# Performance work log

Measured on AMD Instinct MI355X. Metric: run time of the kernel, lower is better.

Reference implementation:

```python
import jax, jax.numpy as jnp
import numpy as np

B, N, C = 8, 8192, 256
H, D, S = 8, 32, 32          # heads, dim_head, slice_num
HID = 4 * C                  # mlp hidden


def layernorm(x, w, b, eps=1e-5):
    mu = jnp.mean(x, axis=-1, keepdims=True)
    var = jnp.mean(jnp.square(x - mu), axis=-1, keepdims=True)
    return (x - mu) * jax.lax.rsqrt(var + eps) * w + b


def setup_inputs() -> dict:
    key = jax.random.key(0)
    ks = jax.random.split(key, 16)
    s = lambda fan: 1.0 / np.sqrt(fan)
    return {
        "fx": jax.random.normal(ks[0], (B, N, C), jnp.float32),
        "ln1_w": jnp.ones((C,), jnp.float32),
        "ln1_b": jnp.zeros((C,), jnp.float32),
        "Wx": jax.random.uniform(ks[1], (C, C), jnp.float32, -s(C), s(C)),   # in_project_x weight [inner,dim]
        "bx": jax.random.uniform(ks[2], (C,), jnp.float32, -s(C), s(C)),
        "Wq": jax.random.uniform(ks[3], (S, D), jnp.float32, -s(D), s(D)),
        "Wk": jax.random.uniform(ks[4], (S, D), jnp.float32, -s(D), s(D)),
        "Wv": jax.random.uniform(ks[5], (D, D), jnp.float32, -s(D), s(D)),
        "Wo": jax.random.uniform(ks[6], (C, C), jnp.float32, -s(C), s(C)),   # to_out weight [dim,inner]
        "bo": jax.random.uniform(ks[7], (C,), jnp.float32, -s(C), s(C)),
        "ln2_w": jnp.ones((C,), jnp.float32),
        "ln2_b": jnp.zeros((C,), jnp.float32),
        "W1": jax.random.uniform(ks[8], (HID, C), jnp.float32, -s(C), s(C)),
        "b1": jax.random.uniform(ks[9], (HID,), jnp.float32, -s(C), s(C)),
        "W2": jax.random.uniform(ks[10], (C, HID), jnp.float32, -s(HID), s(HID)),
        "b2": jax.random.uniform(ks[11], (C,), jnp.float32, -s(HID), s(HID)),
    }


def linear_no_attn(x, Wx, bx, Wq, Wk, Wv, Wo, bo):
    # x: [B,N,C]
    x_mid = x @ Wx.T + bx                                   # [B,N,C]
    x_mid = x_mid.reshape(x.shape[0], x.shape[1], H, D).transpose(0, 2, 1, 3)  # [B,H,N,D]
    q = jax.nn.softmax(x_mid @ Wq.T, axis=-1)               # [B,H,N,S], softmax over slices
    k = jax.nn.softmax(x_mid @ Wk.T, axis=-2)               # [B,H,N,S], softmax over tokens
    v = x_mid @ Wv.T                                        # [B,H,N,D]
    kv = jnp.einsum('bhns,bhnd->bhsd', k, v)                # [B,H,S,D]
    qkv = jnp.einsum('bhns,bhsd->bhnd', q, kv)              # [B,H,N,D]
    qkv = qkv.transpose(0, 2, 1, 3).reshape(x.shape[0], x.shape[1], H * D)
    return qkv @ Wo.T + bo


def reference(fx, ln1_w, ln1_b, Wx, bx, Wq, Wk, Wv, Wo, bo, ln2_w, ln2_b, W1, b1, W2, b2):
    h = linear_no_attn(layernorm(fx, ln1_w, ln1_b), Wx, bx, Wq, Wk, Wv, Wo, bo) + fx
    y = layernorm(h, ln2_w, ln2_b)
    y = jax.nn.gelu(y @ W1.T + b1, approximate=False)       # MLP: pre + exact GELU, n_layers=0
    y = y @ W2.T + b2
    return y + h
```

## Files before the change

### kernel.cpp

```cpp
#include <hip/hip_runtime.h>
#include <math.h>


typedef __attribute__((ext_vector_type(8))) short bf8;
typedef __attribute__((ext_vector_type(4))) float f32x4;
typedef __attribute__((ext_vector_type(4))) unsigned short u16x4;
typedef __attribute__((ext_vector_type(8))) unsigned short u16x8;

__device__ __forceinline__ float b2f(unsigned short x) {
  union { unsigned u; float f; } t; t.u = ((unsigned)x) << 16; return t.f;
}
__device__ __forceinline__ unsigned short f2b(float f) {
  union { float f; unsigned u; } t; t.f = f;
  unsigned r = t.u + 0x7fffu + ((t.u >> 16) & 1u);
  return (unsigned short)(r >> 16);
}
__device__ __forceinline__ float gelu_exact(float x) {
  return 0.5f * x * (1.0f + erff(x * 0.7071067811865475f));
}
__device__ __forceinline__ float erf_fast(float x) {
  float ax = fabsf(x);
  float t = __builtin_amdgcn_rcpf(fmaf(0.3275911f, ax, 1.0f));
  float p = t * fmaf(t, fmaf(t, fmaf(t, fmaf(t, 1.061405429f, -1.453152027f),
                                     1.421413741f), -0.284496736f), 0.254829592f);
  float r = 1.0f - p * __expf(-ax * ax);
  return copysignf(r, x);
}
__device__ __forceinline__ float gelu_fast(float x) {
  return 0.5f * x * (1.0f + erf_fast(x * 0.7071067811865475f));
}

typedef __attribute__((address_space(1))) const void gas_void;
typedef __attribute__((address_space(3))) void las_void;
__device__ __forceinline__ void gl_lds16(const void* g, void* l) {
  __builtin_amdgcn_global_load_lds((gas_void*)g, (las_void*)l, 16, 0, 0);
}

__global__ void sniff_kernel(const unsigned* __restrict__ fx, int* __restrict__ flag) {
  if (threadIdx.x == 0) {
    int cnt = 0;
    for (int i = 0; i < 64; i++) {
      unsigned e = (fx[i] >> 7) & 0xFFu;
      cnt += (e >= 117u && e <= 130u) ? 1 : 0;
    }
    *flag = (cnt >= 32) ? 1 : 0;
  }
}

struct CvtDesc { const void* src[15]; int off[15]; int n[15]; };

__global__ __launch_bounds__(256) void cvt_tab(CvtDesc d, unsigned short* __restrict__ wtab,
                                               const int* __restrict__ flagp) {
  const int seg = blockIdx.y;
  const int i = blockIdx.x * 256 + threadIdx.x;
  if (i >= d.n[seg]) return;
  unsigned short o;
  if (*flagp) o = ((const unsigned short*)d.src[seg])[i];
  else        o = f2b(((const float*)d.src[seg])[i]);
  wtab[d.off[seg] + i] = o;
}

__global__ __launch_bounds__(256) void build_big(
    const unsigned short* __restrict__ wq, const unsigned short* __restrict__ wk,
    unsigned short* __restrict__ Wqbig, unsigned short* __restrict__ Wkbig)
{
  const int idx = blockIdx.x * 256 + threadIdx.x;
  const int row = idx >> 8, col = idx & 255;
  const bool same = (row >> 5) == (col >> 5);
  const int wi = (row & 31) * 32 + (col & 31);
  Wqbig[idx] = same ? wq[wi] : (unsigned short)0;
  Wkbig[idx] = same ? wk[wi] : (unsigned short)0;
}

__global__ __launch_bounds__(256) void zero_u16(unsigned short* __restrict__ p, int n) {
  int i8 = (blockIdx.x * 256 + threadIdx.x) * 8;
  if (i8 < n) { u16x8 z = {}; *(u16x8*)&p[i8] = z; }
}

__global__ __launch_bounds__(256) void ln_stats(
    const void* __restrict__ X, const int* __restrict__ flagp, int amode,
    float* __restrict__ MU, float* __restrict__ RS)
{
  const int lane = threadIdx.x & 63;
  const int wave = threadIdx.x >> 6;
  const size_t row = (size_t)blockIdx.x * 4 + wave;
  const size_t base = row * 256 + lane * 4;
  const bool abf = amode ? ((*flagp) != 0) : true;
  float x0, x1, x2, x3;
  if (abf) {
    u16x4 uv = *(const u16x4*)&((const unsigned short*)X)[base];
    x0 = b2f(uv[0]); x1 = b2f(uv[1]); x2 = b2f(uv[2]); x3 = b2f(uv[3]);
  } else {
    f32x4 t = *(const f32x4*)&((const float*)X)[base];
    x0 = t[0]; x1 = t[1]; x2 = t[2]; x3 = t[3];
  }
  float s = x0 + x1 + x2 + x3;
  float q = x0*x0 + x1*x1 + x2*x2 + x3*x3;
  #pragma unroll
  for (int m = 1; m < 64; m <<= 1) { s += __shfl_xor(s, m, 64); q += __shfl_xor(q, m, 64); }
  float mean = s * (1.0f / 256.0f);
  float var  = q * (1.0f / 256.0f) - mean * mean;
  if (lane == 0) { MU[row] = mean; RS[row] = rsqrtf(var + 1e-5f); }
}

__global__ __launch_bounds__(256) void gemm_bt(
    const unsigned short* __restrict__ A,
    const unsigned short* __restrict__ W,
    const unsigned short* __restrict__ bias,
    const void* __restrict__ Res, const int* __restrict__ flagp,
    unsigned short* __restrict__ Y,
    int N, int K, int act, int mz, long wz)
{
  __shared__ __align__(16) unsigned short smem[3 * 8192];
  const int tid = threadIdx.x, lane = tid & 63, wave = tid >> 6;
  const size_t zrow = (size_t)blockIdx.z * mz;
  const int bm = blockIdx.x * 128, bn = blockIdx.y * 128;
  const int wm = (wave >> 1) * 64, wn = (wave & 1) * 64;
  const int quad = lane >> 4, l16 = lane & 15;
  const unsigned short* Wz = W + (size_t)blockIdx.z * wz;

  f32x4 acc[4][4] = {};
  const int r0 = tid >> 2;
  const int co = (tid & 3) * 8;
  const unsigned short* pa0 = &A[(zrow + bm + r0) * K + co];
  const unsigned short* pa1 = &A[(zrow + bm + r0 + 64) * K + co];
  const unsigned short* pb0 = &Wz[(size_t)(bn + r0) * K + co];
  const unsigned short* pb1 = &Wz[(size_t)(bn + r0 + 64) * K + co];
  const int nt = K >> 5;

  auto stage = [&](int t, int sl) {
    const int k0 = t << 5;
    unsigned short* b_ = &smem[sl * 8192 + tid * 8];
    gl_lds16(pa0 + k0, b_);
    gl_lds16(pa1 + k0, b_ + 2048);
    gl_lds16(pb0 + k0, b_ + 4096);
    gl_lds16(pb1 + k0, b_ + 6144);
  };

  stage(0, 0);
  if (nt > 1) stage(1, 1);
  int scur = 0, snew = 2;
  for (int t = 0; t < nt; ++t) {
    if (t + 2 < nt) {
      stage(t + 2, snew);
      asm volatile("s_waitcnt vmcnt(8)" ::: "memory");
    } else if (t + 1 < nt) {
      asm volatile("s_waitcnt vmcnt(4)" ::: "memory");
    } else {
      asm volatile("s_waitcnt vmcnt(0)" ::: "memory");
    }
    __builtin_amdgcn_s_barrier();
    __builtin_amdgcn_sched_barrier(0);

    const unsigned short* sa = &smem[scur * 8192];
    const unsigned short* sb = sa + 4096;
    bf8 af[4], bfr[4];
    #pragma unroll
    for (int i = 0; i < 4; i++) af[i]  = *(const bf8*)&sa[(wm + i * 16 + l16) * 32 + quad * 8];
    #pragma unroll
    for (int j = 0; j < 4; j++) bfr[j] = *(const bf8*)&sb[(wn + j * 16 + l16) * 32 + quad * 8];
    #pragma unroll
    for (int i = 0; i < 4; i++)
      #pragma unroll
      for (int j = 0; j < 4; j++)
        acc[i][j] = __builtin_amdgcn_mfma_f32_16x16x32_bf16(af[i], bfr[j], acc[i][j], 0, 0, 0);

    __builtin_amdgcn_sched_barrier(0);
    __builtin_amdgcn_s_barrier();
    scur = scur + 1 < 3 ? scur + 1 : 0;
    snew = snew + 1 < 3 ? snew + 1 : 0;
  }

  const bool rbf = Res ? ((*flagp) != 0) : true;
  float bv[4];
  #pragma unroll
  for (int j = 0; j < 4; j++) bv[j] = b2f(bias[bn + wn + j * 16 + l16]);
  #pragma unroll
  for (int i = 0; i < 4; i++)
    #pragma unroll
    for (int j = 0; j < 4; j++)
      #pragma unroll
      for (int r = 0; r < 4; r++) {
        float v = acc[i][j][r] + bv[j];
        if (act == 2) v = __expf(v);
        acc[i][j][r] = v;
      }
  if (act == 3) {
    #pragma unroll
    for (int i = 0; i < 4; i++)
      #pragma unroll
      for (int g = 0; g < 2; g++)
        #pragma unroll
        for (int r = 0; r < 4; r++) {
          float a0 = acc[i][2*g][r], a1 = acc[i][2*g+1][r];
          float m = fmaxf(a0, a1);
          #pragma unroll
          for (int msk = 1; msk < 16; msk <<= 1) m = fmaxf(m, __shfl_xor(m, msk, 64));
          float e0 = __expf(a0 - m), e1 = __expf(a1 - m);
          float s = e0 + e1;
          #pragma unroll
          for (int msk = 1; msk < 16; msk <<= 1) s += __shfl_xor(s, msk, 64);
          const float rz = 1.0f / s;
          acc[i][2*g][r] = e0 * rz; acc[i][2*g+1][r] = e1 * rz;
        }
  }

  float* cf = (float*)smem;
  const int whalf = wm >> 6;
  #pragma unroll
  for (int half = 0; half < 2; ++half) {
    __builtin_amdgcn_s_barrier();
    if (whalf == half) {
      #pragma unroll
      for (int i = 0; i < 4; i++)
        #pragma unroll
        for (int j = 0; j < 4; j++)
          #pragma unroll
          for (int r = 0; r < 4; r++)
            cf[(i * 16 + quad * 4 + r) * 128 + wn + j * 16 + l16] = acc[i][j][r];
    }
    __builtin_amdgcn_s_barrier();
    #pragma unroll
    for (int st = 0; st < 4; ++st) {
      const int e = st * 2048 + tid * 8;
      const int row = e >> 7;
      const size_t gbase = (zrow + bm + half * 64 + row) * (size_t)N + bn + (e & 127);
      float v[8];
      #pragma unroll
      for (int u = 0; u < 8; u++) v[u] = cf[e + u];
      if (Res) {
        if (rbf) {
          u16x8 rv = *(const u16x8*)&((const unsigned short*)Res)[gbase];
          #pragma unroll
          for (int u = 0; u < 8; u++) v[u] += b2f(rv[u]);
        } else {
          f32x4 ra = *(const f32x4*)&((const float*)Res)[gbase];
          f32x4 rb = *(const f32x4*)&((const float*)Res)[gbase + 4];
          v[0] += ra[0]; v[1] += ra[1]; v[2] += ra[2]; v[3] += ra[3];
          v[4] += rb[0]; v[5] += rb[1]; v[6] += rb[2]; v[7] += rb[3];
        }
      }
      u16x8 o;
      #pragma unroll
      for (int u = 0; u < 8; u++) o[u] = f2b(v[u]);
      *(u16x8*)&Y[gbase] = o;
    }
  }
}

__global__ __launch_bounds__(256) void gemm_bt_ln(
    const void* __restrict__ A, const int* __restrict__ flagp, int amode,
    const float* __restrict__ MU, const float* __restrict__ RS,
    const unsigned short* __restrict__ lw, const unsigned short* __restrict__ lb,
    const unsigned short* __restrict__ W, const unsigned short* __restrict__ bias,
    unsigned short* __restrict__ Y, int N, int K, int act)
{
  __shared__ __align__(16) unsigned char smemc[32768];
  unsigned short* lA = (unsigned short*)smemc;
  unsigned short* lB = lA + 4096;
  const int tid = threadIdx.x, lane = tid & 63, wave = tid >> 6;
  const int bm = blockIdx.x * 128, bn = blockIdx.y * 128;
  const int wm = (wave >> 1) * 64, wn = (wave & 1) * 64;
  const int quad = lane >> 4, l16 = lane & 15;
  const bool abf = amode ? ((*flagp) != 0) : true;
  const unsigned short* Ab = (const unsigned short*)A;
  const float* Af = (const float*)A;

  f32x4 acc[4][4] = {};
  const int r0 = tid >> 2;
  const int co = (tid & 3) * 8;
  const unsigned short* pb0 = &W[(size_t)(bn + r0) * K + co];
  const unsigned short* pb1 = &W[(size_t)(bn + r0 + 64) * K + co];

  for (int k0 = 0; k0 < K; k0 += 32) {
    u16x8 wv8 = *(const u16x8*)&lw[k0 + co];
    u16x8 bv8 = *(const u16x8*)&lb[k0 + co];
    __syncthreads();
    gl_lds16(pb0 + k0, &lB[tid * 8]);
    gl_lds16(pb1 + k0, &lB[2048 + tid * 8]);
    #pragma unroll
    for (int half = 0; half < 2; half++) {
      const int ar = bm + r0 + half * 64;
      const float m_ = MU[ar], r_ = RS[ar];
      float xv[8];
      if (abf) {
        u16x8 t = *(const u16x8*)&Ab[(size_t)ar * K + k0 + co];
        #pragma unroll
        for (int e = 0; e < 8; e++) xv[e] = b2f(t[e]);
      } else {
        f32x4 t0 = *(const f32x4*)&Af[(size_t)ar * K + k0 + co];
        f32x4 t1 = *(const f32x4*)&Af[(size_t)ar * K + k0 + co + 4];
        xv[0]=t0[0]; xv[1]=t0[1]; xv[2]=t0[2]; xv[3]=t0[3];
        xv[4]=t1[0]; xv[5]=t1[1]; xv[6]=t1[2]; xv[7]=t1[3];
      }
      u16x8 o;
      #pragma unroll
      for (int e = 0; e < 8; e++)
        o[e] = f2b((xv[e] - m_) * r_ * b2f(wv8[e]) + b2f(bv8[e]));
      *(u16x8*)&lA[half * 2048 + tid * 8] = o;
    }
    __syncthreads();

    bf8 af[4], bfr[4];
    #pragma unroll
    for (int i = 0; i < 4; i++) af[i]  = *(const bf8*)&lA[(wm + i * 16 + l16) * 32 + quad * 8];
    #pragma unroll
    for (int j = 0; j < 4; j++) bfr[j] = *(const bf8*)&lB[(wn + j * 16 + l16) * 32 + quad * 8];
    #pragma unroll
    for (int i = 0; i < 4; i++)
      #pragma unroll
      for (int j = 0; j < 4; j++)
        acc[i][j] = __builtin_amdgcn_mfma_f32_16x16x32_bf16(af[i], bfr[j], acc[i][j], 0, 0, 0);
  }

  float bv[4];
  #pragma unroll
  for (int j = 0; j < 4; j++) bv[j] = b2f(bias[bn + wn + j * 16 + l16]);
  #pragma unroll
  for (int i = 0; i < 4; i++)
    #pragma unroll
    for (int j = 0; j < 4; j++)
      #pragma unroll
      for (int r = 0; r < 4; r++) {
        float v = acc[i][j][r] + bv[j];
        if (act) v = gelu_exact(v);
        acc[i][j][r] = v;
      }

  float* cf = (float*)smemc;
  const int whalf = wm >> 6;
  #pragma unroll
  for (int half = 0; half < 2; ++half) {
    __syncthreads();
    if (whalf == half) {
      #pragma unroll
      for (int i = 0; i < 4; i++)
        #pragma unroll
        for (int j = 0; j < 4; j++)
          #pragma unroll
          for (int r = 0; r < 4; r++)
            cf[(i * 16 + quad * 4 + r) * 128 + wn + j * 16 + l16] = acc[i][j][r];
    }
    __syncthreads();
    #pragma unroll
    for (int st = 0; st < 4; ++st) {
      const int e = st * 2048 + tid * 8;
      const int row = e >> 7;
      const size_t gbase = (size_t)(bm + half * 64 + row) * N + bn + (e & 127);
      u16x8 o;
      #pragma unroll
      for (int u = 0; u < 8; u++) o[u] = f2b(cf[e + u]);
      *(u16x8*)&Y[gbase] = o;
    }
  }
}

__global__ __launch_bounds__(256) void fused_mlp(
    const unsigned short* __restrict__ Hsrc,
    const float* __restrict__ MU, const float* __restrict__ RS,
    const unsigned short* __restrict__ lw, const unsigned short* __restrict__ lb,
    const unsigned short* __restrict__ W1, const unsigned short* __restrict__ bs1,
    const unsigned short* __restrict__ W2, const unsigned short* __restrict__ bs2,
    void* __restrict__ OUT, const int* __restrict__ flagp, long row0)
{
  __shared__ __align__(16) unsigned char smem[70656];
  const int tid = threadIdx.x, lane = tid & 63, wave = tid >> 6;
  const int quad = lane >> 4, l16 = lane & 15;
  const int brow = blockIdx.x * 64;

  auto stageW1 = [&](int c, int b) {
    const unsigned short* src = W1 + (size_t)c * 8192;
    unsigned char* dst = smem + b * 16384;
    #pragma unroll
    for (int s = 0; s < 4; s++) {
      const int unit = s * 256 + tid;
      const int row = unit >> 5, u = unit & 31;
      gl_lds16(src + row * 256 + ((u ^ (row & 7)) * 8), dst + unit * 16);
    }
  };
  auto stageW2 = [&](int c, int b) {
    const unsigned short* src = W2 + c * 32;
    unsigned char* dst = smem + 32768 + b * 16384;
    #pragma unroll
    for (int s = 0; s < 4; s++) {
      const int unit = s * 256 + tid;
      const int row = unit >> 2, u = unit & 3;
      gl_lds16(src + (size_t)row * 1024 + ((u ^ ((row >> 1) & 3)) * 8), dst + unit * 16);
    }
  };

  stageW1(0, 0);
  stageW2(0, 0);

  const int myrow = wave * 16 + l16;
  const float m_ = MU[brow + myrow], r_ = RS[brow + myrow];
  const unsigned short* hr = Hsrc + (size_t)(brow + myrow) * 256 + quad * 8;
  bf8 areg[8];
  #pragma unroll
  for (int ks = 0; ks < 8; ks++) {
    u16x8 hv = *(const u16x8*)&hr[ks * 32];
    u16x8 wv = *(const u16x8*)&lw[ks * 32 + quad * 8];
    u16x8 bv = *(const u16x8*)&lb[ks * 32 + quad * 8];
    u16x8 o;
    #pragma unroll
    for (int e = 0; e < 8; e++)
      o[e] = f2b((b2f(hv[e]) - m_) * r_ * b2f(wv[e]) + b2f(bv[e]));
    *(u16x8*)&areg[ks] = o;
  }

  asm volatile("s_waitcnt vmcnt(0)" ::: "memory");
  __builtin_amdgcn_s_barrier();

  f32x4 acc[16] = {};
  unsigned short* tw = (unsigned short*)(smem + 65536 + wave * 1280);
  const int gsw = (l16 >> 1) & 3;
  int bsel = 0;

  for (int c = 0; c < 32; ++c) {
    if (c + 1 < 32) {
      stageW1(c + 1, bsel ^ 1);
      stageW2(c + 1, bsel ^ 1);
      __builtin_amdgcn_sched_barrier(0);
    }

    const unsigned short* w1b = (const unsigned short*)(smem + bsel * 16384);
    f32x4 p0 = {}, p1 = {};
    #pragma unroll
    for (int ks = 0; ks < 8; ks++) {
      const int slot = (ks * 4 + quad) ^ (l16 & 7);
      bf8 a0, a1;
      *(u16x8*)&a0 = *(const u16x8*)&w1b[l16 * 256 + slot * 8];
      *(u16x8*)&a1 = *(const u16x8*)&w1b[(16 + l16) * 256 + slot * 8];
      p0 = __builtin_amdgcn_mfma_f32_16x16x32_bf16(a0, areg[ks], p0, 0, 0, 0);
      p1 = __builtin_amdgcn_mfma_f32_16x16x32_bf16(a1, areg[ks], p1, 0, 0, 0);
    }

    {
      u16x4 bv0 = *(const u16x4*)&bs1[c * 32 + quad * 4];
      u16x4 bv1 = *(const u16x4*)&bs1[c * 32 + 16 + quad * 4];
      u16x4 o0, o1;
      #pragma unroll
      for (int r = 0; r < 4; r++) {
        o0[r] = f2b(gelu_fast(p0[r] + b2f(bv0[r])));
        o1[r] = f2b(gelu_fast(p1[r] + b2f(bv1[r])));
      }
      *(u16x4*)&tw[l16 * 40 + quad * 4]      = o0;
      *(u16x4*)&tw[l16 * 40 + 16 + quad * 4] = o1;
    }
    asm volatile("s_waitcnt lgkmcnt(0)" ::: "memory");
    __builtin_amdgcn_sched_barrier(0);

    bf8 ta;
    *(u16x8*)&ta = *(const u16x8*)&tw[l16 * 40 + quad * 8];
    const unsigned short* w2b = (const unsigned short*)(smem + 32768 + bsel * 16384);
    #pragma unroll
    for (int j = 0; j < 16; j++) {
      bf8 bw;
      *(u16x8*)&bw = *(const u16x8*)&w2b[(j * 16 + l16) * 32 + ((quad ^ gsw) * 8)];
      acc[j] = __builtin_amdgcn_mfma_f32_16x16x32_bf16(ta, bw, acc[j], 0, 0, 0);
    }

    asm volatile("s_waitcnt vmcnt(0)" ::: "memory");
    __builtin_amdgcn_s_barrier();
    bsel ^= 1;
  }

  float* cf = (float*)smem;
  #pragma unroll
  for (int j = 0; j < 16; j++)
    #pragma unroll
    for (int r = 0; r < 4; r++)
      cf[(wave * 16 + quad * 4 + r) * 256 + j * 16 + l16] = acc[j][r];
  __syncthreads();

  const bool obf = (*flagp) != 0;
  const unsigned short* hrow = Hsrc + (size_t)brow * 256;
  #pragma unroll
  for (int s = 0; s < 8; s++) {
    const int e = s * 2048 + tid * 8;
    const int row = e >> 8, col = e & 255;
    u16x8 rv = *(const u16x8*)&hrow[e];
    u16x8 b2v = *(const u16x8*)&bs2[col];
    float v[8];
    #pragma unroll
    for (int u = 0; u < 8; u++) v[u] = cf[e + u] + b2f(rv[u]) + b2f(b2v[u]);
    const size_t ob = (size_t)(row0 + brow + row) * 256 + col;
    if (obf) {
      u16x8 o;
      #pragma unroll
      for (int u = 0; u < 8; u++) o[u] = f2b(v[u]);
      *(u16x8*)&((unsigned short*)OUT)[ob] = o;
    } else {
      f32x4 oa, obv;
      oa[0]=v[0]; oa[1]=v[1]; oa[2]=v[2]; oa[3]=v[3];
      obv[0]=v[4]; obv[1]=v[5]; obv[2]=v[6]; obv[3]=v[7];
      *(f32x4*)&((float*)OUT)[ob] = oa;
      *(f32x4*)&((float*)OUT)[ob + 4] = obv;
    }
  }
}

__global__ __launch_bounds__(256) void accumG(
    const unsigned short* __restrict__ X,
    const unsigned short* __restrict__ E,
    float* __restrict__ Gp)
{
  __shared__ float Xl[64 * 256];
  __shared__ __align__(16) unsigned short El[64 * 256];
  const int tid = threadIdx.x;
  const int k = blockIdx.x;
  const int h = tid >> 5, s = tid & 31;

  float acc[32];
  #pragma unroll
  for (int d = 0; d < 32; d++) acc[d] = 0.f;
  float zacc = 0.f;

  for (int sub = 0; sub < 4; sub++) {
    const size_t r0s = (size_t)k * 256 + sub * 64;
    __syncthreads();
    #pragma unroll
    for (int i = 0; i < 8; i++) {
      const int flat = i * 2048 + tid * 8;
      u16x8 xv = *(const u16x8*)&X[r0s * 256 + flat];
      #pragma unroll
      for (int e = 0; e < 8; e++) Xl[flat + e] = b2f(xv[e]);
      *(u16x8*)&El[flat] = *(const u16x8*)&E[r0s * 256 + flat];
    }
    __syncthreads();

    for (int t = 0; t < 64; t++) {
      const float e = b2f(El[t * 256 + h * 32 + s]);
      zacc += e;
      const int xb = t * 256 + h * 32;
      #pragma unroll
      for (int dq = 0; dq < 8; dq++) {
        f32x4 xv = *(const f32x4*)&Xl[xb + dq * 4];
        acc[dq*4+0] += e * xv[0];
        acc[dq*4+1] += e * xv[1];
        acc[dq*4+2] += e * xv[2];
        acc[dq*4+3] += e * xv[3];
      }
    }
  }

  float* gp = &Gp[(size_t)k * 8448 + (size_t)tid * 32];
  #pragma unroll
  for (int dq = 0; dq < 8; dq++) {
    f32x4 o; o[0]=acc[dq*4]; o[1]=acc[dq*4+1]; o[2]=acc[dq*4+2]; o[3]=acc[dq*4+3];
    *(f32x4*)&gp[dq * 4] = o;
  }
  Gp[(size_t)k * 8448 + 8192 + tid] = zacc;
}

__global__ __launch_bounds__(256) void reduceG(const float* __restrict__ Gp,
                                               float* __restrict__ Gfin) {
  const int o = blockIdx.x * 256 + threadIdx.x;
  if (o >= 67584) return;
  const int b = o / 8448;
  const int j = o - b * 8448;
  float s = 0.f;
  #pragma unroll 8
  for (int i = 0; i < 32; i++) s += Gp[(size_t)(b * 32 + i) * 8448 + j];
  Gfin[o] = s;
}

__global__ __launch_bounds__(256) void kv_build(
    const float* __restrict__ Gfin, const unsigned short* __restrict__ Wv,
    unsigned short* __restrict__ KVB)
{
  __shared__ float Gl[8192];
  __shared__ float zl[256];
  __shared__ float wvt[1024];
  const int tid = threadIdx.x;
  const int b = blockIdx.x;
  for (int i = tid; i < 8192; i += 256) Gl[i] = Gfin[(size_t)b * 8448 + i];
  zl[tid] = Gfin[(size_t)b * 8448 + 8192 + tid];
  for (int i = tid; i < 1024; i += 256) {
    const int dd = i >> 5, d = i & 31;
    wvt[i] = b2f(Wv[d * 32 + dd]);
  }
  __syncthreads();

  const int h = tid >> 5, d = tid & 31;
  unsigned short row[32];
  for (int s = 0; s < 32; s++) {
    float a = 0.f;
    #pragma unroll
    for (int dd = 0; dd < 32; dd++) a += Gl[h * 1024 + s * 32 + dd] * wvt[dd * 32 + d];
    row[s] = f2b(a / zl[h * 32 + s]);
  }
  unsigned short* out = &KVB[(size_t)b * 65536 + (size_t)(h * 32 + d) * 256 + h * 32];
  #pragma unroll
  for (int e = 0; e < 4; e++) *(u16x8*)&out[e * 8] = *(u16x8*)&row[e * 8];
}

__global__ __launch_bounds__(256) void copy_h0(const unsigned short* __restrict__ src,
                                               unsigned short* __restrict__ dst) {
  size_t i = ((size_t)blockIdx.x * 256 + threadIdx.x) * 8;
  *(u16x8*)&dst[i] = *(const u16x8*)&src[i];
}

extern "C" void kernel_launch(void* const* d_in, const int* in_sizes, int n_in,
                              void* d_out, int out_size, void* d_ws, size_t ws_size,
                              hipStream_t stream)
{
  const void* fx   = d_in[0];
  const void* ln1w = d_in[1];
  const void* ln1b = d_in[2];
  const void* Wx   = d_in[3];
  const void* bx   = d_in[4];
  const void* Wq   = d_in[5];
  const void* Wk   = d_in[6];
  const void* Wv   = d_in[7];
  const void* Wo   = d_in[8];
  const void* bo   = d_in[9];
  const void* ln2w = d_in[10];
  const void* ln2b = d_in[11];
  const void* W1   = d_in[12];
  const void* b1   = d_in[13];
  const void* W2   = d_in[14];
  const void* b2   = d_in[15];

  unsigned short* ws    = (unsigned short*)d_ws;
  unsigned short* hid   = ws;
  float* Gp             = (float*)ws;
  unsigned short* wtab  = ws + 8388608;
  unsigned short* h0res = wtab + 661248;
  float* Gfin           = (float*)h0res;
  unsigned short* Wqbig = h0res + 2097152;
  unsigned short* Wkbig = Wqbig + 65536;
  unsigned short* KVB   = Wkbig + 65536;
  unsigned short* zbias = KVB + 524288;
  float* fpw = (float*)(zbias + 256);
  float* mu1 = fpw;
  float* rs1 = fpw + 65536;
  float* mu2 = fpw + 131072;
  float* rs2 = fpw + 196608;
  int* flagp = (int*)(fpw + 262144);

  const int OFF_LN1W=0, OFF_LN1B=256, OFF_WX=512, OFF_BX=66048,
            OFF_WQ=66304, OFF_WK=67328, OFF_WV=68352,
            OFF_WO=69376, OFF_BO=134912, OFF_LN2W=135168, OFF_LN2B=135424,
            OFF_W1=135680, OFF_B1=397824, OFF_W2=398848, OFF_B2=660992;

  unsigned short* xm  = (unsigned short*)d_out;
  unsigned short* xup = xm + 16777216;

  sniff_kernel<<<1, 64, 0, stream>>>((const unsigned*)fx, flagp);
  CvtDesc cd;
  const void* srcs[15] = {ln1w, ln1b, Wx, bx, Wq, Wk, Wv, Wo, bo, ln2w, ln2b, W1, b1, W2, b2};
  const int offs[15]   = {OFF_LN1W, OFF_LN1B, OFF_WX, OFF_BX, OFF_WQ, OFF_WK, OFF_WV,
                          OFF_WO, OFF_BO, OFF_LN2W, OFF_LN2B, OFF_W1, OFF_B1, OFF_W2, OFF_B2};
  const int ns[15]     = {256, 256, 65536, 256, 1024, 1024, 1024, 65536, 256, 256, 256,
                          262144, 1024, 262144, 256};
  for (int i = 0; i < 15; i++) { cd.src[i] = srcs[i]; cd.off[i] = offs[i]; cd.n[i] = ns[i]; }
  cvt_tab<<<dim3(1024, 15), 256, 0, stream>>>(cd, wtab, flagp);
  build_big<<<256, 256, 0, stream>>>(wtab + OFF_WQ, wtab + OFF_WK, Wqbig, Wkbig);
  zero_u16<<<257, 256, 0, stream>>>(KVB, 524544);

  ln_stats<<<16384, 256, 0, stream>>>(fx, flagp, 1, mu1, rs1);
  gemm_bt_ln<<<dim3(512, 2), 256, 0, stream>>>(fx, flagp, 1, mu1, rs1,
      wtab + OFF_LN1W, wtab + OFF_LN1B, wtab + OFF_WX, wtab + OFF_BX,
      xm, 256, 256, 0);

  gemm_bt<<<dim3(512, 2), 256, 0, stream>>>(xm, Wkbig, zbias, nullptr, flagp,
                                            xup, 256, 256, 2, 0, 0);

  accumG<<<256, 256, 0, stream>>>(xm, xup, Gp);
  reduceG<<<264, 256, 0, stream>>>(Gp, Gfin);
  kv_build<<<8, 256, 0, stream>>>(Gfin, wtab + OFF_WV, KVB);

  gemm_bt<<<dim3(512, 2), 256, 0, stream>>>(xm, Wqbig, zbias, nullptr, flagp,
                                            xup, 256, 256, 3, 0, 0);

  gemm_bt<<<dim3(64, 2, 8), 256, 0, stream>>>(xup, KVB, zbias, nullptr, flagp,
                                              xm, 256, 256, 0, 8192, 65536);

  gemm_bt<<<dim3(512, 2), 256, 0, stream>>>(xm, wtab + OFF_WO, wtab + OFF_BO, fx, flagp,
                                            xup, 256, 256, 0, 0, 0);

  ln_stats<<<16384, 256, 0, stream>>>(xup, flagp, 0, mu2, rs2);
  copy_h0<<<4096, 256, 0, stream>>>(xup + (size_t)32768 * 256, hid);

  fused_mlp<<<512, 256, 0, stream>>>(xup, mu2, rs2,
      wtab + OFF_LN2W, wtab + OFF_LN2B, wtab + OFF_W1, wtab + OFF_B1,
      wtab + OFF_W2, wtab + OFF_B2, d_out, flagp, 0L);
  fused_mlp<<<512, 256, 0, stream>>>(hid, mu2 + 32768, rs2 + 32768,
      wtab + OFF_LN2W, wtab + OFF_LN2B, wtab + OFF_W1, wtab + OFF_B1,
      wtab + OFF_W2, wtab + OFF_B2, d_out, flagp, 32768L);
}
```

Baseline: 487.4 us.

## Double rows per fused MLP block to reuse staged weights across two row groups

The fused MLP kernel now handles 128 rows per block instead of 64. Each wave computes two 16-row groups against the same staged W1/W2 tiles, which halves the weight-staging traffic per row and raises MFMA work per LDS load. The b1 bias is cached in LDS, the epilogue is split into two halves with padded row stride, and the GEMM epilogue stride is padded to 132 to avoid bank conflicts. In exchange, register pressure goes up (launch bounds set to 1 block), LDS usage grows, and grid size halves to 256 blocks, which may underfill the CUs.

```diff
diff --git a/kernel.cpp b/kernel.cpp
--- a/kernel.cpp
+++ b/kernel.cpp
@@ -217,17 +217,18 @@
         for (int j = 0; j < 4; j++)
           #pragma unroll
           for (int r = 0; r < 4; r++)
-            cf[(i * 16 + quad * 4 + r) * 128 + wn + j * 16 + l16] = acc[i][j][r];
+            cf[(i * 16 + quad * 4 + r) * 132 + wn + j * 16 + l16] = acc[i][j][r];
     }
     __builtin_amdgcn_s_barrier();
     #pragma unroll
     for (int st = 0; st < 4; ++st) {
       const int e = st * 2048 + tid * 8;
       const int row = e >> 7;
-      const size_t gbase = (zrow + bm + half * 64 + row) * (size_t)N + bn + (e & 127);
+      const int col = e & 127;
+      const size_t gbase = (zrow + bm + half * 64 + row) * (size_t)N + bn + col;
       float v[8];
       #pragma unroll
-      for (int u = 0; u < 8; u++) v[u] = cf[e + u];
+      for (int u = 0; u < 8; u++) v[u] = cf[row * 132 + col + u];
       if (Res) {
         if (rbf) {
           u16x8 rv = *(const u16x8*)&((const unsigned short*)Res)[gbase];
@@ -355,7 +356,7 @@
   }
 }
 
-__global__ __launch_bounds__(256) void fused_mlp(
+__global__ __launch_bounds__(256, 1) void fused_mlp(
     const unsigned short* __restrict__ Hsrc,
     const float* __restrict__ MU, const float* __restrict__ RS,
     const unsigned short* __restrict__ lw, const unsigned short* __restrict__ lb,
@@ -363,10 +364,10 @@
     const unsigned short* __restrict__ W2, const unsigned short* __restrict__ bs2,
     void* __restrict__ OUT, const int* __restrict__ flagp, long row0)
 {
-  __shared__ __align__(16) unsigned char smem[70656];
+  __shared__ __align__(16) unsigned char smem[77824];
   const int tid = threadIdx.x, lane = tid & 63, wave = tid >> 6;
   const int quad = lane >> 4, l16 = lane & 15;
-  const int brow = blockIdx.x * 64;
+  const int brow = blockIdx.x * 128;
 
   auto stageW1 = [&](int c, int b) {
     const unsigned short* src = W1 + (size_t)c * 8192;
@@ -392,27 +393,34 @@
   stageW1(0, 0);
   stageW2(0, 0);
 
-  const int myrow = wave * 16 + l16;
-  const float m_ = MU[brow + myrow], r_ = RS[brow + myrow];
-  const unsigned short* hr = Hsrc + (size_t)(brow + myrow) * 256 + quad * 8;
-  bf8 areg[8];
-  #pragma unroll
-  for (int ks = 0; ks < 8; ks++) {
-    u16x8 hv = *(const u16x8*)&hr[ks * 32];
-    u16x8 wv = *(const u16x8*)&lw[ks * 32 + quad * 8];
-    u16x8 bv = *(const u16x8*)&lb[ks * 32 + quad * 8];
-    u16x8 o;
-    #pragma unroll
-    for (int e = 0; e < 8; e++)
-      o[e] = f2b((b2f(hv[e]) - m_) * r_ * b2f(wv[e]) + b2f(bv[e]));
-    *(u16x8*)&areg[ks] = o;
-  }
-
-  asm volatile("s_waitcnt vmcnt(0)" ::: "memory");
+  unsigned short* b1l = (unsigned short*)(smem + 75776);
+  if (tid < 128) *(u16x8*)&b1l[tid * 8] = *(const u16x8*)&bs1[tid * 8];
+
+  bf8 areg[2][8];
+  #pragma unroll
+  for (int rg = 0; rg < 2; rg++) {
+    const int myrow = wave * 32 + rg * 16 + l16;
+    const float m_ = MU[brow + myrow], r_ = RS[brow + myrow];
+    const unsigned short* hr = Hsrc + (size_t)(brow + myrow) * 256 + quad * 8;
+    #pragma unroll
+    for (int ks = 0; ks < 8; ks++) {
+      u16x8 hv = *(const u16x8*)&hr[ks * 32];
+      u16x8 wv = *(const u16x8*)&lw[ks * 32 + quad * 8];
+      u16x8 bv = *(const u16x8*)&lb[ks * 32 + quad * 8];
+      u16x8 o;
+      #pragma unroll
+      for (int e = 0; e < 8; e++)
+        o[e] = f2b((b2f(hv[e]) - m_) * r_ * b2f(wv[e]) + b2f(bv[e]));
+      *(u16x8*)&areg[rg][ks] = o;
+    }
+  }
+
+  asm volatile("s_waitcnt vmcnt(0) lgkmcnt(0)" ::: "memory");
   __builtin_amdgcn_s_barrier();
-
-  f32x4 acc[16] = {};
-  unsigned short* tw = (unsigned short*)(smem + 65536 + wave * 1280);
+  __builtin_amdgcn_sched_barrier(0);
+
+  f32x4 acc[2][16] = {};
+  unsigned short* tw = (unsigned short*)(smem + 65536 + wave * 2560);
   const int gsw = (l16 >> 1) & 3;
   int bsel = 0;
 
@@ -424,78 +432,95 @@
     }
 
     const unsigned short* w1b = (const unsigned short*)(smem + bsel * 16384);
-    f32x4 p0 = {}, p1 = {};
+    f32x4 p00 = {}, p01 = {}, p10 = {}, p11 = {};
     #pragma unroll
     for (int ks = 0; ks < 8; ks++) {
       const int slot = (ks * 4 + quad) ^ (l16 & 7);
       bf8 a0, a1;
       *(u16x8*)&a0 = *(const u16x8*)&w1b[l16 * 256 + slot * 8];
       *(u16x8*)&a1 = *(const u16x8*)&w1b[(16 + l16) * 256 + slot * 8];
-      p0 = __builtin_amdgcn_mfma_f32_16x16x32_bf16(a0, areg[ks], p0, 0, 0, 0);
-      p1 = __builtin_amdgcn_mfma_f32_16x16x32_bf16(a1, areg[ks], p1, 0, 0, 0);
+      p00 = __builtin_amdgcn_mfma_f32_16x16x32_bf16(a0, areg[0][ks], p00, 0, 0, 0);
+      p01 = __builtin_amdgcn_mfma_f32_16x16x32_bf16(a0, areg[1][ks], p01, 0, 0, 0);
+      p10 = __builtin_amdgcn_mfma_f32_16x16x32_bf16(a1, areg[0][ks], p10, 0, 0, 0);
+      p11 = __builtin_amdgcn_mfma_f32_16x16x32_bf16(a1, areg[1][ks], p11, 0, 0, 0);
     }
 
     {
-      u16x4 bv0 = *(const u16x4*)&bs1[c * 32 + quad * 4];
-      u16x4 bv1 = *(const u16x4*)&bs1[c * 32 + 16 + quad * 4];
-      u16x4 o0, o1;
+      u16x4 bv0 = *(const u16x4*)&b1l[c * 32 + quad * 4];
+      u16x4 bv1 = *(const u16x4*)&b1l[c * 32 + 16 + quad * 4];
+      u16x4 o00, o01, o10, o11;
       #pragma unroll
       for (int r = 0; r < 4; r++) {
-        o0[r] = f2b(gelu_fast(p0[r] + b2f(bv0[r])));
-        o1[r] = f2b(gelu_fast(p1[r] + b2f(bv1[r])));
+        o00[r] = f2b(gelu_fast(p00[r] + b2f(bv0[r])));
+        o01[r] = f2b(gelu_fast(p01[r] + b2f(bv0[r])));
+        o10[r] = f2b(gelu_fast(p10[r] + b2f(bv1[r])));
+        o11[r] = f2b(gelu_fast(p11[r] + b2f(bv1[r])));
       }
-      *(u16x4*)&tw[l16 * 40 + quad * 4]      = o0;
-      *(u16x4*)&tw[l16 * 40 + 16 + quad * 4] = o1;
+      *(u16x4*)&tw[l16 * 40 + quad * 4]             = o00;
+      *(u16x4*)&tw[(16 + l16) * 40 + quad * 4]      = o01;
+      *(u16x4*)&tw[l16 * 40 + 16 + quad * 4]        = o10;
+      *(u16x4*)&tw[(16 + l16) * 40 + 16 + quad * 4] = o11;
     }
     asm volatile("s_waitcnt lgkmcnt(0)" ::: "memory");
     __builtin_amdgcn_sched_barrier(0);
 
-    bf8 ta;
-    *(u16x8*)&ta = *(const u16x8*)&tw[l16 * 40 + quad * 8];
+    bf8 ta0, ta1;
+    *(u16x8*)&ta0 = *(const u16x8*)&tw[l16 * 40 + quad * 8];
+    *(u16x8*)&ta1 = *(const u16x8*)&tw[(16 + l16) * 40 + quad * 8];
     const unsigned short* w2b = (const unsigned short*)(smem + 32768 + bsel * 16384);
     #pragma unroll
     for (int j = 0; j < 16; j++) {
       bf8 bw;
       *(u16x8*)&bw = *(const u16x8*)&w2b[(j * 16 + l16) * 32 + ((quad ^ gsw) * 8)];
-      acc[j] = __builtin_amdgcn_mfma_f32_16x16x32_bf16(ta, bw, acc[j], 0, 0, 0);
+      acc[0][j] = __builtin_amdgcn_mfma_f32_16x16x32_bf16(ta0, bw, acc[0][j], 0, 0, 0);
+      acc[1][j] = __builtin_amdgcn_mfma_f32_16x16x32_bf16(ta1, bw, acc[1][j], 0, 0, 0);
     }
 
     asm volatile("s_waitcnt vmcnt(0)" ::: "memory");
     __builtin_amdgcn_s_barrier();
+    __builtin_amdgcn_sched_barrier(0);
     bsel ^= 1;
   }
 
+  const bool obf = (*flagp) != 0;
   float* cf = (float*)smem;
   #pragma unroll
-  for (int j = 0; j < 16; j++)
-    #pragma unroll
-    for (int r = 0; r < 4; r++)
-      cf[(wave * 16 + quad * 4 + r) * 256 + j * 16 + l16] = acc[j][r];
-  __syncthreads();
-
-  const bool obf = (*flagp) != 0;
-  const unsigned short* hrow = Hsrc + (size_t)brow * 256;
-  #pragma unroll
-  for (int s = 0; s < 8; s++) {
-    const int e = s * 2048 + tid * 8;
-    const int row = e >> 8, col = e & 255;
-    u16x8 rv = *(const u16x8*)&hrow[e];
-    u16x8 b2v = *(const u16x8*)&bs2[col];
-    float v[8];
-    #pragma unroll
-    for (int u = 0; u < 8; u++) v[u] = cf[e + u] + b2f(rv[u]) + b2f(b2v[u]);
-    const size_t ob = (size_t)(row0 + brow + row) * 256 + col;
-    if (obf) {
-      u16x8 o;
-      #pragma unroll
-      for (int u = 0; u < 8; u++) o[u] = f2b(v[u]);
-      *(u16x8*)&((unsigned short*)OUT)[ob] = o;
-    } else {
-      f32x4 oa, obv;
-      oa[0]=v[0]; oa[1]=v[1]; oa[2]=v[2]; oa[3]=v[3];
-      obv[0]=v[4]; obv[1]=v[5]; obv[2]=v[6]; obv[3]=v[7];
-      *(f32x4*)&((float*)OUT)[ob] = oa;
-      *(f32x4*)&((float*)OUT)[ob + 4] = obv;
+  for (int h = 0; h < 2; ++h) {
+    __syncthreads();
+    if ((wave >> 1) == h) {
+      const int wl = (wave & 1) * 32;
+      #pragma unroll
+      for (int rg = 0; rg < 2; rg++)
+        #pragma unroll
+        for (int j = 0; j < 16; j++)
+          #pragma unroll
+          for (int r = 0; r < 4; r++)
+            cf[(wl + rg * 16 + quad * 4 + r) * 260 + j * 16 + l16] = acc[rg][j][r];
+    }
+    __syncthreads();
+    const unsigned short* hrow = Hsrc + (size_t)(brow + h * 64) * 256;
+    #pragma unroll
+    for (int s = 0; s < 8; s++) {
+      const int e = s * 2048 + tid * 8;
+      const int row = e >> 8, col = e & 255;
+      u16x8 rv = *(const u16x8*)&hrow[e];
+      u16x8 b2v = *(const u16x8*)&bs2[col];
+      float v[8];
+      #pragma unroll
+      for (int u = 0; u < 8; u++) v[u] = cf[row * 260 + col + u] + b2f(rv[u]) + b2f(b2v[u]);
+      const size_t ob = (size_t)(row0 + brow + h * 64 + row) * 256 + col;
+      if (obf) {
+        u16x8 o;
+        #pragma unroll
+        for (int u = 0; u < 8; u++) o[u] = f2b(v[u]);
+        *(u16x8*)&((unsigned short*)OUT)[ob] = o;
+      } else {
+        f32x4 oa, obv;
+        oa[0]=v[0]; oa[1]=v[1]; oa[2]=v[2]; oa[3]=v[3];
+        obv[0]=v[4]; obv[1]=v[5]; obv[2]=v[6]; obv[3]=v[7];
+        *(f32x4*)&((float*)OUT)[ob] = oa;
+        *(f32x4*)&((float*)OUT)[ob + 4] = obv;
+      }
     }
   }
 }
@@ -683,10 +708,10 @@
   ln_stats<<<16384, 256, 0, stream>>>(xup, flagp, 0, mu2, rs2);
   copy_h0<<<4096, 256, 0, stream>>>(xup + (size_t)32768 * 256, hid);
 
-  fused_mlp<<<512, 256, 0, stream>>>(xup, mu2, rs2,
+  fused_mlp<<<256, 256, 0, stream>>>(xup, mu2, rs2,
       wtab + OFF_LN2W, wtab + OFF_LN2B, wtab + OFF_W1, wtab + OFF_B1,
       wtab + OFF_W2, wtab + OFF_B2, d_out, flagp, 0L);
-  fused_mlp<<<512, 256, 0, stream>>>(hid, mu2 + 32768, rs2 + 32768,
+  fused_mlp<<<256, 256, 0, stream>>>(hid, mu2 + 32768, rs2 + 32768,
       wtab + OFF_LN2W, wtab + OFF_LN2B, wtab + OFF_W1, wtab + OFF_B1,
       wtab + OFF_W2, wtab + OFF_B2, d_out, flagp, 32768L);
 }
```

Result: no change. 492.9 us (+1.1%).
